# Kernel optimization log

Measured on AMD Instinct MI355X. Metric: run time of the kernel, lower is better.

Reference implementation:

```python
import jax, jax.numpy as jnp
import numpy as np

B, AT, NBR, FEAT = 4, 384, 24, 128


def setup_inputs() -> dict:
    key = jax.random.key(0)
    k1, k2, k3 = jax.random.split(key, 3)
    edge_embedding = jax.random.normal(k1, (B, AT, NBR, FEAT), dtype=jnp.float32)
    nbr_idx = jax.random.randint(k2, (B, AT, NBR), 0, AT, dtype=jnp.int64)
    # periodic-cell offsets: small integers stored as float, compared exactly with ==
    cell_offset = jax.random.randint(k3, (B, AT, NBR, 3), 0, 3).astype(jnp.float32)
    return {"edge_embedding": edge_embedding, "nbr_idx": nbr_idx, "cell_offset": cell_offset}


def reference(edge_embedding, nbr_idx, cell_offset):
    # edge_embedding: (B, At, Nbr, F); nbr_idx: (B, At, Nbr) int; cell_offset: (B, At, Nbr, 3)
    Bn, At, Nbr, F = edge_embedding.shape

    # j_nbr[b,a,j,k] = nbr_idx[b, nbr_idx[b,a,j], k]  -- neighbors of atom j (j-th nbr of a)
    j_nbr = jax.vmap(lambda n: n[n])(nbr_idx)                      # (B, At, Nbr, Nbr)
    # cell_j[b,a,j,k,:] = cell_offset[b, nbr_idx[b,a,j], k, :]
    cell_j = jax.vmap(lambda c, n: c[n])(cell_offset, nbr_idx)     # (B, At, Nbr, Nbr, 3)

    # k_masked[b,a,j,i] = nbr_idx[b,a,i] with diagonal (i==j) set to -1 (exclude k==j)
    eye = jnp.eye(Nbr, dtype=bool)                                 # (Nbr, Nbr) [j, i]
    k_masked = jnp.where(eye[None, None], -1, nbr_idx[:, :, None, :])  # (B, At, Nbr, Nbr)

    # match over k: j_nbr[b,a,j,k] == k_masked[b,a,j,i]
    idx_eq = j_nbr[:, :, :, None, :] == k_masked[:, :, :, :, None]      # (B,At,Nbr,Nbr_i,Nbr_k)
    # cell check: cell_offset[b,a,i,:] == cell_j[b,a,j,k,:] for all 3 coords
    cell_eq = jnp.all(
        cell_offset[:, :, None, :, None, :] == cell_j[:, :, :, None, :, :],
        axis=-1,
    )                                                              # (B,At,Nbr,Nbr_i,Nbr_k)

    mask = jnp.any(idx_eq & cell_eq, axis=-1)                      # (B, At, Nbr_j, Nbr_i)

    # edge_jk[b,a,j,i,:] = edge_embedding[b,a,i,:] where mask else 0
    edge_jk = jnp.where(mask[..., None], edge_embedding[:, :, None, :, :],
                        jnp.zeros((), dtype=edge_embedding.dtype))
    return edge_jk
```

## Files before the change

### kernel.cpp

```cpp
#include <hip/hip_runtime.h>

#define Bb 4
#define AT 384
#define NBR 24
#define FEAT 128
#define ROWQ (FEAT / 4)
#define PANELQ (NBR * ROWQ)

__global__ __launch_bounds__(256) void GetEdgeJK_kernel(
    const float4* __restrict__ edge,
    const int*    __restrict__ nbr,
    const float*  __restrict__ cell,
    float4*       __restrict__ out)
{
    const int ba = blockIdx.x;
    const int b  = ba / AT;
    const int t  = threadIdx.x;

    __shared__ int   s_nbr[NBR];
    __shared__ float s_cell[NBR][3];
    __shared__ int   s_nbrj[NBR][NBR];
    __shared__ float s_cellj[NBR][NBR][3];
    __shared__ int   s_mask[NBR * NBR];

    if (t < NBR) {
        s_nbr[t]     = nbr[ba * NBR + t];
        s_cell[t][0] = cell[(ba * NBR + t) * 3 + 0];
        s_cell[t][1] = cell[(ba * NBR + t) * 3 + 1];
        s_cell[t][2] = cell[(ba * NBR + t) * 3 + 2];
    }
    __syncthreads();

    for (int q = t; q < NBR * NBR; q += 256) {
        const int j = q / NBR;
        const int k = q % NBR;
        const int base = (b * AT + s_nbr[j]) * NBR + k;
        s_nbrj[j][k]     = nbr[base];
        s_cellj[j][k][0] = cell[base * 3 + 0];
        s_cellj[j][k][1] = cell[base * 3 + 1];
        s_cellj[j][k][2] = cell[base * 3 + 2];
    }
    __syncthreads();

    for (int p = t; p < NBR * NBR; p += 256) {
        const int j = p / NBR;
        const int i = p % NBR;
        int m = 0;
        if (i != j) {
            const int   myidx = s_nbr[i];
            const float c0 = s_cell[i][0];
            const float c1 = s_cell[i][1];
            const float c2 = s_cell[i][2];
            #pragma unroll
            for (int k = 0; k < NBR; ++k) {
                if (s_nbrj[j][k] == myidx &&
                    s_cellj[j][k][0] == c0 &&
                    s_cellj[j][k][1] == c1 &&
                    s_cellj[j][k][2] == c2) { m = 1; }
            }
        }
        s_mask[p] = m;
    }
    __syncthreads();

    const float4* __restrict__ erow = edge + (size_t)ba * PANELQ;
    float4*       __restrict__ orow = out  + (size_t)ba * NBR * PANELQ;
    const float4 zero = make_float4(0.f, 0.f, 0.f, 0.f);

    for (int j = 0; j < NBR; ++j) {
        const int* __restrict__ mrow = &s_mask[j * NBR];
        #pragma unroll
        for (int it = 0; it < 3; ++it) {
            const int q = it * 256 + t;
            const int i = q >> 5;
            float4 v = zero;
            if (mrow[i]) v = erow[q];
            orow[j * PANELQ + q] = v;
        }
    }
}

extern "C" void kernel_launch(void* const* d_in, const int* in_sizes, int n_in,
                              void* d_out, int out_size, void* d_ws, size_t ws_size,
                              hipStream_t stream) {
    const float4* edge = (const float4*)d_in[0];
    const int*    nbr  = (const int*)d_in[1];
    const float*  cell = (const float*)d_in[2];
    float4*       out  = (float4*)d_out;

    const int nblocks = Bb * AT;
    GetEdgeJK_kernel<<<nblocks, 256, 0, stream>>>(edge, nbr, cell, out);
}
```

Measured before the change: 100.3 us.

## Split output into bulk zero-fill kernel and sparse scatter of masked rows

```diff
diff --git a/kernel.cpp b/kernel.cpp
--- a/kernel.cpp
+++ b/kernel.cpp
@@ -6,12 +6,25 @@
 #define FEAT 128
 #define ROWQ (FEAT / 4)
 #define PANELQ (NBR * ROWQ)
+#define OUTQ ((size_t)Bb * AT * NBR * NBR * ROWQ)
 
-__global__ __launch_bounds__(256) void GetEdgeJK_kernel(
-    const float4* __restrict__ edge,
-    const int*    __restrict__ nbr,
-    const float*  __restrict__ cell,
-    float4*       __restrict__ out)
+typedef float vfloat4 __attribute__((ext_vector_type(4)));
+
+__global__ __launch_bounds__(256) void fill_kernel(
+    vfloat4* __restrict__ out, unsigned int n)
+{
+    const vfloat4 zero = (vfloat4)(0.f);
+    unsigned int idx = blockIdx.x * 256u + threadIdx.x;
+    const unsigned int stride = gridDim.x * 256u;
+    for (; idx < n; idx += stride)
+        out[idx] = zero;
+}
+
+__global__ __launch_bounds__(256) void scatter_kernel(
+    const vfloat4* __restrict__ edge,
+    const int*     __restrict__ nbr,
+    const float*   __restrict__ cell,
+    vfloat4*       __restrict__ out)
 {
     const int ba = blockIdx.x;
     const int b  = ba / AT;
@@ -21,8 +34,10 @@
     __shared__ float s_cell[NBR][3];
     __shared__ int   s_nbrj[NBR][NBR];
     __shared__ float s_cellj[NBR][NBR][3];
-    __shared__ int   s_mask[NBR * NBR];
+    __shared__ int   s_list[NBR * NBR];
+    __shared__ int   s_cnt;
 
+    if (t == 0) s_cnt = 0;
     if (t < NBR) {
         s_nbr[t]     = nbr[ba * NBR + t];
         s_cell[t][0] = cell[(ba * NBR + t) * 3 + 0];
@@ -45,12 +60,12 @@
     for (int p = t; p < NBR * NBR; p += 256) {
         const int j = p / NBR;
         const int i = p % NBR;
-        int m = 0;
         if (i != j) {
             const int   myidx = s_nbr[i];
             const float c0 = s_cell[i][0];
             const float c1 = s_cell[i][1];
             const float c2 = s_cell[i][2];
+            int m = 0;
             #pragma unroll
             for (int k = 0; k < NBR; ++k) {
                 if (s_nbrj[j][k] == myidx &&
@@ -58,36 +73,35 @@
                     s_cellj[j][k][1] == c1 &&
                     s_cellj[j][k][2] == c2) { m = 1; }
             }
+            if (m) {
+                const int slot = atomicAdd(&s_cnt, 1);
+                s_list[slot] = (j << 5) | i;
+            }
         }
-        s_mask[p] = m;
     }
     __syncthreads();
 
-    const float4* __restrict__ erow = edge + (size_t)ba * PANELQ;
-    float4*       __restrict__ orow = out  + (size_t)ba * NBR * PANELQ;
-    const float4 zero = make_float4(0.f, 0.f, 0.f, 0.f);
-
-    for (int j = 0; j < NBR; ++j) {
-        const int* __restrict__ mrow = &s_mask[j * NBR];
-        #pragma unroll
-        for (int it = 0; it < 3; ++it) {
-            const int q = it * 256 + t;
-            const int i = q >> 5;
-            float4 v = zero;
-            if (mrow[i]) v = erow[q];
-            orow[j * PANELQ + q] = v;
-        }
+    const int cnt  = s_cnt;
+    const int g    = t >> 5;
+    const int lane = t & 31;
+    const vfloat4* __restrict__ erow = edge + (size_t)ba * PANELQ;
+    for (int p = g; p < cnt; p += 8) {
+        const int ji = s_list[p];
+        const int j  = ji >> 5;
+        const int i  = ji & 31;
+        const vfloat4 v = erow[i * ROWQ + lane];
+        out[((size_t)(ba * NBR + j) * NBR + i) * ROWQ + lane] = v;
     }
 }
 
 extern "C" void kernel_launch(void* const* d_in, const int* in_sizes, int n_in,
                               void* d_out, int out_size, void* d_ws, size_t ws_size,
                               hipStream_t stream) {
-    const float4* edge = (const float4*)d_in[0];
-    const int*    nbr  = (const int*)d_in[1];
-    const float*  cell = (const float*)d_in[2];
-    float4*       out  = (float4*)d_out;
+    const vfloat4* edge = (const vfloat4*)d_in[0];
+    const int*     nbr  = (const int*)d_in[1];
+    const float*   cell = (const float*)d_in[2];
+    vfloat4*       out  = (vfloat4*)d_out;
 
-    const int nblocks = Bb * AT;
-    GetEdgeJK_kernel<<<nblocks, 256, 0, stream>>>(edge, nbr, cell, out);
+    fill_kernel<<<2048, 256, 0, stream>>>(out, (unsigned int)OUTQ);
+    scatter_kernel<<<Bb * AT, 256, 0, stream>>>(edge, nbr, cell, out);
 }
```

Result: slower. 118.4 us (+18.0%).
